# Kernel tuning notes

Measured on AMD Instinct MI355X. Metric: run time of the kernel, lower is better.

Reference implementation:

```python
import jax, jax.numpy as jnp
import numpy as np

VOCAB, EMBED, HID, OUT = 32000, 256, 256, 1
B, S = 32, 4096


def setup_inputs() -> dict:
    key = jax.random.key(0)
    ks = jax.random.split(key, 7)
    X = jax.random.randint(ks[0], (B, S), 0, VOCAB, dtype=jnp.int32)
    emb = jax.random.normal(ks[1], (VOCAB, EMBED), dtype=jnp.float32) * 0.02
    # Conv1d(embedding_dim, 3*hidden, kernel_size=1) == pointwise linear
    conv_w = jax.random.normal(ks[2], (3 * HID, EMBED), dtype=jnp.float32) * (1.0 / np.sqrt(EMBED))
    conv_b = jax.random.normal(ks[3], (3 * HID,), dtype=jnp.float32) * 0.01
    Mu = jax.random.normal(ks[4], (HID, 1), dtype=jnp.float32) * (1.0 / np.sqrt(HID))
    W_out = jax.random.normal(ks[5], (OUT, HID), dtype=jnp.float32) * (1.0 / np.sqrt(HID))
    b_out = jax.random.normal(ks[6], (OUT,), dtype=jnp.float32) * 0.01
    return {"X": X, "emb": emb, "conv_w": conv_w, "conv_b": conv_b,
            "Mu": Mu, "W_out": W_out, "b_out": b_out}


def reference(X, emb, conv_w, conv_b, Mu, W_out, b_out):
    # embedding lookup: [B, S, E]
    embedded = emb[X]
    # kernel-size-1 conv == per-token linear E -> 3H
    zfo = jnp.einsum('bse,he->bsh', embedded, conv_w) + conv_b  # [B, S, 3H]
    z, f, o = jnp.split(zfo, 3, axis=2)
    z = jnp.tanh(z)
    f = jax.nn.sigmoid(f)
    # o gate computed but unused in the original forward path

    # linear recurrence h_t = f_t * h_{t-1} + (1 - f_t) * z_t via scan over time
    z_t = jnp.transpose(z, (1, 0, 2))  # [S, B, H]
    f_t = jnp.transpose(f, (1, 0, 2))  # [S, B, H]

    def step(h, zf):
        zt, ft = zf
        h = ft * h + (1.0 - ft) * zt
        return h, h

    h0 = jnp.zeros((X.shape[0], HID), dtype=z.dtype)
    _, hs = jax.lax.scan(step, h0, (z_t, f_t))
    hidden_states = jnp.transpose(hs, (1, 0, 2))  # [B, S, H]

    # attention pooling over seq dim
    attn = jnp.einsum('bsh,hl->bsl', hidden_states, Mu)      # [B, S, 1]
    attn = jax.nn.softmax(attn, axis=1)
    context = jnp.einsum('bsh,bsl->bh', hidden_states, attn)  # [B, H]
    # dropout p=0 -> identity
    output = context @ W_out.T + b_out                        # [B, 1]
    return output
```

## Files before the change

kernel.cpp:

```cpp
#include <hip/hip_runtime.h>
#include <math.h>

#define VOCABN 32000
#define EMBEDN 256
#define HIDN   256
#define BN     32
#define SN     4096
#define CH     32
#define WU     16
#define NCHUNK (SN / CH)

typedef __attribute__((ext_vector_type(8))) _Float16 half8;
typedef __attribute__((ext_vector_type(4))) _Float16 half4;
typedef __attribute__((ext_vector_type(4))) float f32x4;

__global__ __launch_bounds__(256)
void cvt_kernel(const float* __restrict__ s, _Float16* __restrict__ d, int n8) {
    const int i = blockIdx.x * 256 + threadIdx.x;
    if (i < n8) {
        const float4 a = ((const float4*)s)[2 * i];
        const float4 b = ((const float4*)s)[2 * i + 1];
        half8 h;
        h[0] = (_Float16)a.x; h[1] = (_Float16)a.y; h[2] = (_Float16)a.z; h[3] = (_Float16)a.w;
        h[4] = (_Float16)b.x; h[5] = (_Float16)b.y; h[6] = (_Float16)b.z; h[7] = (_Float16)b.w;
        ((half8*)d)[i] = h;
    }
}

__global__ __launch_bounds__(256, 2)
void build_tab_kernel(const float* __restrict__ emb, const _Float16* __restrict__ cwh,
                      const float* __restrict__ cb, _Float16* __restrict__ zf) {
    __shared__ _Float16 As[64 * 264];

    const int t = threadIdx.x, lane = t & 63, wc = t >> 6;
    const int v0   = blockIdx.x * 64;
    const int n    = lane & 15;
    const int kseg = lane >> 4, ko = kseg * 8;

    #pragma unroll
    for (int i = 0; i < 16; ++i) {
        const int idx = t + i * 256;
        const int row = idx >> 6;
        const int k4  = (idx & 63) * 4;
        float4 a = *(const float4*)(emb + (size_t)(v0 + row) * EMBEDN + k4);
        half4 h;
        h[0] = (_Float16)a.x; h[1] = (_Float16)a.y;
        h[2] = (_Float16)a.z; h[3] = (_Float16)a.w;
        *(half4*)(As + row * 264 + k4) = h;
    }

    const _Float16* Aw = cwh + (size_t)(wc * 64 + n) * EMBEDN + ko;
    half8 fw[8], fwn[8];
    #pragma unroll
    for (int a = 0; a < 8; ++a)
        fw[a] = *(const half8*)(Aw + (size_t)((a >> 2) * 256 + (a & 3) * 16) * EMBEDN);

    f32x4 acc[8][4];
    #pragma unroll
    for (int a = 0; a < 8; ++a)
        #pragma unroll
        for (int b = 0; b < 4; ++b) acc[a][b] = (f32x4)0.f;

    __syncthreads();

    #pragma unroll
    for (int k = 0; k < 8; ++k) {
        if (k < 7) {
            #pragma unroll
            for (int a = 0; a < 8; ++a)
                fwn[a] = *(const half8*)(Aw + (size_t)((a >> 2) * 256 + (a & 3) * 16) * EMBEDN
                                            + (k + 1) * 32);
        }
        half8 fv[4];
        #pragma unroll
        for (int b = 0; b < 4; ++b)
            fv[b] = *(const half8*)(As + (b * 16 + n) * 264 + k * 32 + ko);
        #pragma unroll
        for (int a = 0; a < 8; ++a)
            #pragma unroll
            for (int b = 0; b < 4; ++b)
                acc[a][b] = __builtin_amdgcn_mfma_f32_16x16x32_f16(fw[a], fv[b], acc[a][b], 0, 0, 0);
        if (k < 7) {
            #pragma unroll
            for (int a = 0; a < 8; ++a) fw[a] = fwn[a];
        }
    }

    const int chq = wc * 64 + kseg * 4;
    #pragma unroll
    for (int ct = 0; ct < 4; ++ct) {
        const f32x4 bz = *(const f32x4*)(cb + chq + ct * 16);
        const f32x4 bf = *(const f32x4*)(cb + 256 + chq + ct * 16);
        #pragma unroll
        for (int vt = 0; vt < 4; ++vt) {
            const int v = v0 + vt * 16 + n;
            half8 h8;
            #pragma unroll
            for (int r = 0; r < 4; ++r) {
                const float x  = acc[ct][vt][r] + bz[r];
                const float e  = __expf(2.f * x);
                const float zv = __fdividef(e - 1.f, e + 1.f);
                const float y  = acc[ct + 4][vt][r] + bf[r];
                const float fv2 = __fdividef(1.f, 1.f + __expf(-y));
                h8[2 * r]     = (_Float16)zv;
                h8[2 * r + 1] = (_Float16)fv2;
            }
            *(half8*)(zf + (size_t)v * 512 + (size_t)(chq + ct * 16) * 2) = h8;
        }
    }
}

__global__ __launch_bounds__(256, 4)
void scan_kernel(const int* __restrict__ X, const _Float16* __restrict__ zf,
                 const float* __restrict__ Mu, const float* __restrict__ Wout,
                 float* __restrict__ pbuf) {
    __shared__ int ids[4][CH + WU];
    __shared__ _Float16 hA[4][16][264];

    const int t = threadIdx.x, w = t >> 6, lane = t & 63;
    const int b = blockIdx.y, c = blockIdx.x * 4 + w;
    const int n = lane & 15, kseg = lane >> 4;
    const int sMid = c * CH;
    int sBeg = sMid - WU; if (sBeg < 0) sBeg = 0;
    const int nWarm = sMid - sBeg;
    const int nTot  = nWarm + CH;

    for (int i = lane; i < nTot; i += 64) ids[w][i] = X[(size_t)b * SN + sBeg + i];
    __syncthreads();

    half8 fb[8];
    #pragma unroll
    for (int kc = 0; kc < 8; ++kc) {
        #pragma unroll
        for (int j = 0; j < 8; ++j) {
            const int ch = kc * 32 + kseg * 8 + j;
            float v = 0.f;
            if (n == 0) v = Mu[ch];
            else if (n == 1) v = Wout[ch];
            fb[kc][j] = (_Float16)v;
        }
    }

    const _Float16* base = zf + 8 * lane;
    half8 p[8];
    #pragma unroll
    for (int i = 0; i < 8; ++i)
        p[i] = *(const half8*)(base + (size_t)ids[w][i] * 512);

    float h0 = 0.f, h1 = 0.f, h2 = 0.f, h3 = 0.f;
    float se = 0.f, sq = 0.f;
    _Float16* myA = &hA[w][0][0];
    const int nG = nTot >> 4, gWarm = nWarm >> 4;

    for (int gi = 0; gi < nG; ++gi) {
        const bool act = (gi >= gWarm);
        #pragma unroll
        for (int ii = 0; ii < 16; ++ii) {
            const int i = gi * 16 + ii;
            half8 cur = p[ii & 7];
            const int nx = i + 8;
            if (nx < nTot) p[ii & 7] = *(const half8*)(base + (size_t)ids[w][nx] * 512);
            const float z0 = (float)cur[0], f0 = (float)cur[1];
            const float z1 = (float)cur[2], f1 = (float)cur[3];
            const float z2 = (float)cur[4], f2 = (float)cur[5];
            const float z3 = (float)cur[6], f3 = (float)cur[7];
            h0 = z0 + f0 * (h0 - z0);
            h1 = z1 + f1 * (h1 - z1);
            h2 = z2 + f2 * (h2 - z2);
            h3 = z3 + f3 * (h3 - z3);
            if (act) {
                half4 hh;
                hh[0] = (_Float16)h0; hh[1] = (_Float16)h1;
                hh[2] = (_Float16)h2; hh[3] = (_Float16)h3;
                *(half4*)(myA + ii * 264 + 4 * lane) = hh;
            }
        }
        if (act) {
            f32x4 a4 = (f32x4)0.f;
            #pragma unroll
            for (int kc = 0; kc < 8; ++kc) {
                half8 fa = *(const half8*)(myA + n * 264 + kc * 32 + kseg * 8);
                a4 = __builtin_amdgcn_mfma_f32_16x16x32_f16(fa, fb[kc], a4, 0, 0, 0);
            }
            const float q0 = __shfl_xor(a4[0], 1);
            const float q1 = __shfl_xor(a4[1], 1);
            const float q2 = __shfl_xor(a4[2], 1);
            const float q3 = __shfl_xor(a4[3], 1);
            const float e0 = __expf(a4[0]), e1 = __expf(a4[1]);
            const float e2 = __expf(a4[2]), e3 = __expf(a4[3]);
            se += (e0 + e1) + (e2 + e3);
            sq += (e0 * q0 + e1 * q1) + (e2 * q2 + e3 * q3);
        }
    }

    se += __shfl_xor(se, 16); sq += __shfl_xor(sq, 16);
    se += __shfl_xor(se, 32); sq += __shfl_xor(sq, 32);
    if (lane == 0)
        *(float2*)&pbuf[(size_t)(b * NCHUNK + c) * 2] = make_float2(se, sq);
}

__global__ __launch_bounds__(64)
void pool_kernel(const float* __restrict__ pbuf, const float* __restrict__ bout,
                 float* __restrict__ out) {
    const int b = blockIdx.x, t = threadIdx.x;
    float se = 0.f, sq = 0.f;
    #pragma unroll
    for (int i = 0; i < 2; ++i) {
        const float2 p = *(const float2*)&pbuf[(size_t)(b * NCHUNK + t + i * 64) * 2];
        se += p.x; sq += p.y;
    }
    #pragma unroll
    for (int off = 32; off; off >>= 1) { se += __shfl_xor(se, off); sq += __shfl_xor(sq, off); }
    if (t == 0) out[b] = sq / se + bout[0];
}

extern "C" void kernel_launch(void* const* d_in, const int* in_sizes, int n_in,
                              void* d_out, int out_size, void* d_ws, size_t ws_size,
                              hipStream_t stream) {
    const int*   X    = (const int*)d_in[0];
    const float* emb  = (const float*)d_in[1];
    const float* cw   = (const float*)d_in[2];
    const float* cb   = (const float*)d_in[3];
    const float* Mu   = (const float*)d_in[4];
    const float* Wout = (const float*)d_in[5];
    const float* bout = (const float*)d_in[6];
    float* out = (float*)d_out;

    _Float16* cwh  = (_Float16*)d_ws;
    _Float16* zf   = cwh + (size_t)512 * EMBEDN;
    float*    pbuf = (float*)(zf + (size_t)VOCABN * 512);

    const int nCw8 = 512 * EMBEDN / 8;
    cvt_kernel<<<(nCw8 + 255) / 256, 256, 0, stream>>>(cw, cwh, nCw8);
    build_tab_kernel<<<VOCABN / 64, 256, 0, stream>>>(emb, cwh, cb, zf);
    scan_kernel<<<dim3(NCHUNK / 4, BN), 256, 0, stream>>>(X, zf, Mu, Wout, pbuf);
    pool_kernel<<<BN, 64, 0, stream>>>(pbuf, bout, out);
}
```

Measured before the change: 151.0 us.

## Fold (1-f)*z into the table, double the scan chunk and prefetch depth

The table build now stores (1-f)*z in place of z, so each recurrence step becomes a single FMA (h = f*h + a). The scan chunk grows from 32 to 64 tokens, halving the share of warm-up overhead per chunk and the number of partial sums the pool kernel reduces. The gather prefetch depth doubles from 8 to 16 rows to hide more memory latency. The wider prefetch uses more registers, so launch bounds drop to 2 blocks per SM, and the larger chunks also mean fewer blocks overall.

```diff
diff --git a/kernel.cpp b/kernel.cpp
--- a/kernel.cpp
+++ b/kernel.cpp
@@ -6,7 +6,7 @@
 #define HIDN   256
 #define BN     32
 #define SN     4096
-#define CH     32
+#define CH     64
 #define WU     16
 #define NCHUNK (SN / CH)
 
@@ -102,7 +102,7 @@
                 const float zv = __fdividef(e - 1.f, e + 1.f);
                 const float y  = acc[ct + 4][vt][r] + bf[r];
                 const float fv2 = __fdividef(1.f, 1.f + __expf(-y));
-                h8[2 * r]     = (_Float16)zv;
+                h8[2 * r]     = (_Float16)(zv * (1.f - fv2));
                 h8[2 * r + 1] = (_Float16)fv2;
             }
             *(half8*)(zf + (size_t)v * 512 + (size_t)(chq + ct * 16) * 2) = h8;
@@ -110,7 +110,7 @@
     }
 }
 
-__global__ __launch_bounds__(256, 4)
+__global__ __launch_bounds__(256, 2)
 void scan_kernel(const int* __restrict__ X, const _Float16* __restrict__ zf,
                  const float* __restrict__ Mu, const float* __restrict__ Wout,
                  float* __restrict__ pbuf) {
@@ -119,7 +119,8 @@
 
     const int t = threadIdx.x, w = t >> 6, lane = t & 63;
     const int b = blockIdx.y, c = blockIdx.x * 4 + w;
-    const int n = lane & 15, kseg = lane >> 4;
+    const int n = lane & 15, kseg = lane >> 6 ? 0 : (lane >> 4);
+    const int ks = lane >> 4;
     const int sMid = c * CH;
     int sBeg = sMid - WU; if (sBeg < 0) sBeg = 0;
     const int nWarm = sMid - sBeg;
@@ -133,7 +134,7 @@
     for (int kc = 0; kc < 8; ++kc) {
         #pragma unroll
         for (int j = 0; j < 8; ++j) {
-            const int ch = kc * 32 + kseg * 8 + j;
+            const int ch = kc * 32 + ks * 8 + j;
             float v = 0.f;
             if (n == 0) v = Mu[ch];
             else if (n == 1) v = Wout[ch];
@@ -142,9 +143,9 @@
     }
 
     const _Float16* base = zf + 8 * lane;
-    half8 p[8];
-    #pragma unroll
-    for (int i = 0; i < 8; ++i)
+    half8 p[16];
+    #pragma unroll
+    for (int i = 0; i < 16; ++i)
         p[i] = *(const half8*)(base + (size_t)ids[w][i] * 512);
 
     float h0 = 0.f, h1 = 0.f, h2 = 0.f, h3 = 0.f;
@@ -157,17 +158,17 @@
         #pragma unroll
         for (int ii = 0; ii < 16; ++ii) {
             const int i = gi * 16 + ii;
-            half8 cur = p[ii & 7];
-            const int nx = i + 8;
-            if (nx < nTot) p[ii & 7] = *(const half8*)(base + (size_t)ids[w][nx] * 512);
-            const float z0 = (float)cur[0], f0 = (float)cur[1];
-            const float z1 = (float)cur[2], f1 = (float)cur[3];
-            const float z2 = (float)cur[4], f2 = (float)cur[5];
-            const float z3 = (float)cur[6], f3 = (float)cur[7];
-            h0 = z0 + f0 * (h0 - z0);
-            h1 = z1 + f1 * (h1 - z1);
-            h2 = z2 + f2 * (h2 - z2);
-            h3 = z3 + f3 * (h3 - z3);
+            half8 cur = p[ii];
+            const int nx = i + 16;
+            if (nx < nTot) p[ii] = *(const half8*)(base + (size_t)ids[w][nx] * 512);
+            const float a0 = (float)cur[0], f0 = (float)cur[1];
+            const float a1 = (float)cur[2], f1 = (float)cur[3];
+            const float a2 = (float)cur[4], f2 = (float)cur[5];
+            const float a3 = (float)cur[6], f3 = (float)cur[7];
+            h0 = f0 * h0 + a0;
+            h1 = f1 * h1 + a1;
+            h2 = f2 * h2 + a2;
+            h3 = f3 * h3 + a3;
             if (act) {
                 half4 hh;
                 hh[0] = (_Float16)h0; hh[1] = (_Float16)h1;
@@ -179,7 +180,7 @@
             f32x4 a4 = (f32x4)0.f;
             #pragma unroll
             for (int kc = 0; kc < 8; ++kc) {
-                half8 fa = *(const half8*)(myA + n * 264 + kc * 32 + kseg * 8);
+                half8 fa = *(const half8*)(myA + n * 264 + kc * 32 + ks * 8);
                 a4 = __builtin_amdgcn_mfma_f32_16x16x32_f16(fa, fb[kc], a4, 0, 0, 0);
             }
             const float q0 = __shfl_xor(a4[0], 1);
@@ -203,12 +204,8 @@
 void pool_kernel(const float* __restrict__ pbuf, const float* __restrict__ bout,
                  float* __restrict__ out) {
     const int b = blockIdx.x, t = threadIdx.x;
-    float se = 0.f, sq = 0.f;
-    #pragma unroll
-    for (int i = 0; i < 2; ++i) {
-        const float2 p = *(const float2*)&pbuf[(size_t)(b * NCHUNK + t + i * 64) * 2];
-        se += p.x; sq += p.y;
-    }
+    const float2 p = *(const float2*)&pbuf[(size_t)(b * NCHUNK + t) * 2];
+    float se = p.x, sq = p.y;
     #pragma unroll
     for (int off = 32; off; off >>= 1) { se += __shfl_xor(se, off); sq += __shfl_xor(sq, off); }
     if (t == 0) out[b] = sq / se + bout[0];
```

After: 148.1 us. About the same (-1.9%).
